# Performance work log

Hardware: AMD Instinct MI355X
Metric: run time of the kernel (lower is better)

## Reference

```python
import jax, jax.numpy as jnp
import numpy as np

EPS = 1e-5


def setup_inputs() -> dict:
    key = jax.random.key(0)
    k1, k2, k3 = jax.random.split(key, 3)
    B, D, T = 16, 256, 4096
    K = 2048
    x = jax.random.normal(k1, (B, D, T), dtype=jnp.float32)
    embedding_sum = jax.random.normal(k2, (K, D), dtype=jnp.float32)
    cluster_usage = jax.random.uniform(k3, (K,), dtype=jnp.float32)
    return {"x": x, "embedding_sum": embedding_sum, "cluster_usage": cluster_usage}


def reference(x, embedding_sum, cluster_usage):
    # embedding property: embedding_sum / clamp(cluster_usage, min=eps)
    emb = embedding_sum / jnp.clip(cluster_usage, EPS, None)[:, None]  # [K, D]
    B, D, T = x.shape
    x_flat = jnp.transpose(x, (0, 2, 1)).reshape(B * T, D)  # (b t) d
    # compute faithfully (clamped for numerical safety).
    x2 = jnp.sum(x_flat * x_flat, axis=-1, keepdims=True)      # [BT, 1]
    e2 = jnp.sum(emb * emb, axis=-1)                           # [K]
    d2 = x2 - 2.0 * (x_flat @ emb.T) + e2[None, :]             # [BT, K]
    distances = jnp.sqrt(jnp.clip(d2, 0.0, None))
    codes = jnp.argmin(distances, axis=-1).reshape(B, 1, T)    # int codes
    # decode: embedding gather, b t d -> b d t
    decoded = jnp.transpose(emb[codes[:, 0, :]], (0, 2, 1))    # [B, D, T]
    return codes, decoded
```

## Files before the change

kernel.cpp:

```cpp
#include <hip/hip_runtime.h>
#include <hip/hip_fp16.h>
#include <cmath>

#define EPS 1e-5f
#define TAU 0.15f
#define RP  8

#define Bn 16
#define Dn 256
#define Tn 4096
#define Kn 2048

typedef unsigned short ushort_t;
typedef __attribute__((ext_vector_type(8))) _Float16 f16x8;
typedef __attribute__((ext_vector_type(4))) float f32x4;

__device__ __forceinline__ unsigned short f2h(float v) {
    return __half_as_ushort(__float2half_rn(v));
}

#define GLOAD_LDS16(gp, lp) __builtin_amdgcn_global_load_lds( \
    (const __attribute__((address_space(1))) unsigned int*)(gp), \
    (__attribute__((address_space(3))) unsigned int*)(lp), 16, 0, 0)

__global__ __launch_bounds__(256) void prep_kernel(
    const float* __restrict__ es, const float* __restrict__ usage,
    float* __restrict__ emb, ushort_t* __restrict__ e16,
    float* __restrict__ bias, float4* __restrict__ embT4,
    int* __restrict__ counter)
{
    __shared__ float sh[256];
    __shared__ float wsum[4];
    const int k = blockIdx.x;
    const int d = threadIdx.x;
    const float inv = 1.0f / fmaxf(usage[k], EPS);
    const float v = es[(size_t)k * Dn + d] * inv;
    emb[(size_t)k * Dn + d] = v;
    e16[(size_t)k * Dn + d] = f2h(fminf(fmaxf(v, -65504.f), 65504.f));
    sh[d] = v;
    float sq = v * v;
    #pragma unroll
    for (int off = 32; off > 0; off >>= 1) sq += __shfl_down(sq, off, 64);
    const int lane = d & 63, wv = d >> 6;
    if (lane == 0) wsum[wv] = sq;
    __syncthreads();
    if (d < 64)
        embT4[(size_t)d * Kn + k] = make_float4(sh[4*d], sh[4*d+1], sh[4*d+2], sh[4*d+3]);
    if (d == 0) {
        bias[k] = 0.5f * (wsum[0] + wsum[1] + wsum[2] + wsum[3]);
        if (k == 0) *counter = 0;
    }
}

#define BARRIER_PIN()                                                         \
    __builtin_amdgcn_s_barrier();                                             \
    __builtin_amdgcn_sched_barrier(0)

#define STAGE_B(dst, kcc, hh)                                                 \
    {                                                                         \
        _Pragma("unroll")                                                     \
        for (int r = 0; r < 4; ++r) {                                         \
            const int c   = r * 512 + tid;                                    \
            const int row = c >> 4;                                           \
            const int col = (((c & 15) ^ (row & 15)) << 3);                   \
            GLOAD_LDS16(e16 + ((size_t)((kcc) * 128 + row)) * Dn + (hh) * 128 + col, \
                        (dst) + ((r * 512 + (wid << 6)) << 3));               \
        }                                                                     \
    }

#define COMPUTE_ACC(bbuf, afArr)                                              \
    {                                                                         \
        __builtin_amdgcn_s_setprio(1);                                        \
        _Pragma("unroll")                                                     \
        for (int ks = 0; ks < 4; ++ks)                                        \
            _Pragma("unroll")                                                 \
            for (int j = 0; j < 8; ++j) {                                     \
                const f16x8 bf = *(const f16x8*)(                             \
                    &(bbuf)[((j << 4) + l15) * 128 +                          \
                            ((((ks << 2) | quad) ^ l15) << 3)]);              \
                _Pragma("unroll")                                             \
                for (int i = 0; i < 2; ++i)                                   \
                    acc[i][j] = __builtin_amdgcn_mfma_f32_16x16x32_f16(       \
                        afArr[ks * 2 + i], bf, acc[i][j], 0, 0, 0);           \
            }                                                                 \
        __builtin_amdgcn_s_setprio(0);                                        \
    }

__global__ __launch_bounds__(512, 2) void gemm_argmax(
    const float* __restrict__ x, const ushort_t* __restrict__ e16,
    const float* __restrict__ bias_g, const float* __restrict__ emb,
    int* __restrict__ codes_i, float* __restrict__ codes_f,
    int* __restrict__ list, int* __restrict__ counter,
    float* __restrict__ decoded)
{
    __shared__ __align__(16) ushort_t BsS[2][128 * 128];
    __shared__ __align__(16) float    biasLds[2048];
    __shared__ int codeLds[256];

    const int bid = blockIdx.x;
    const int b   = bid >> 4;
    const int tt  = bid & 15;
    const int t0  = tt << 8;

    const int tid  = threadIdx.x;
    const int lane = tid & 63;
    const int wid  = tid >> 6;
    const int l15  = lane & 15;
    const int quad = lane >> 4;
    const int wm   = wid;

    const size_t bTt0 = (size_t)b * Tn + t0;

    GLOAD_LDS16(bias_g + (tid << 2), biasLds + (wid << 8));

    f16x8 af0[8], af1[8];
    {
        const float* xb = x + (size_t)b * Dn * Tn;
        #pragma unroll
        for (int ks = 0; ks < 4; ++ks)
            #pragma unroll
            for (int i = 0; i < 2; ++i) {
                const int t = t0 + (wm << 5) + (i << 4) + l15;
                const float* c0 = xb + ((size_t)(ks * 32 + quad * 8)) * Tn + t;
                const float* c1 = c0 + (size_t)128 * Tn;
                f16x8 v0, v1;
                #pragma unroll
                for (int e = 0; e < 8; ++e) {
                    v0[e] = (_Float16)c0[(size_t)e * Tn];
                    v1[e] = (_Float16)c1[(size_t)e * Tn];
                }
                af0[ks * 2 + i] = v0;
                af1[ks * 2 + i] = v1;
            }
    }

    f32x4 acc[2][8];
    float S1[2][4], S2[2][4];
    int   K1[2][4];
    #pragma unroll
    for (int i = 0; i < 2; ++i)
        #pragma unroll
        for (int r = 0; r < 4; ++r) { S1[i][r] = -INFINITY; S2[i][r] = -INFINITY; K1[i][r] = 0; }
    #pragma unroll
    for (int i = 0; i < 2; ++i)
        #pragma unroll
        for (int j = 0; j < 8; ++j)
            acc[i][j] = (f32x4){-INFINITY, -INFINITY, -INFINITY, -INFINITY};

    asm volatile("s_waitcnt vmcnt(0)" ::: "memory");
    BARRIER_PIN();
    STAGE_B(&BsS[0][0], 0, 0);
    STAGE_B(&BsS[1][0], 0, 1);

    #pragma unroll 1
    for (int kc = 0; kc < 16; ++kc) {
        asm volatile("s_waitcnt vmcnt(4)" ::: "memory");
        BARRIER_PIN();
        {
            float bj[8];
            #pragma unroll
            for (int j = 0; j < 8; ++j)
                bj[j] = biasLds[(kc << 7) + (j << 4) + l15];
            const int kdrb = ((kc - 1) << 7) + l15;
            __builtin_amdgcn_s_setprio(1);
            #pragma unroll
            for (int j = 0; j < 8; ++j) {
                const f16x8 bf0 = *(const f16x8*)(
                    &BsS[0][((j << 4) + l15) * 128 + ((quad ^ l15) << 3)]);
                const float nb = -bj[j];
                const f32x4 cin = {nb, nb, nb, nb};
                const int kdr = kdrb + (j << 4);
                #pragma unroll
                for (int i = 0; i < 2; ++i) {
                    #pragma unroll
                    for (int r = 0; r < 4; ++r) {
                        const float s = acc[i][j][r];
                        S2[i][r] = __builtin_amdgcn_fmed3f(s, S1[i][r], S2[i][r]);
                        const bool gt = s > S1[i][r];
                        K1[i][r] = gt ? kdr : K1[i][r];
                        S1[i][r] = fmaxf(S1[i][r], s);
                    }
                    acc[i][j] = __builtin_amdgcn_mfma_f32_16x16x32_f16(
                        af0[i], bf0, cin, 0, 0, 0);
                }
            }
            #pragma unroll
            for (int ks = 1; ks < 4; ++ks)
                #pragma unroll
                for (int j = 0; j < 8; ++j) {
                    const f16x8 bf = *(const f16x8*)(
                        &BsS[0][((j << 4) + l15) * 128 +
                                ((((ks << 2) | quad) ^ l15) << 3)]);
                    #pragma unroll
                    for (int i = 0; i < 2; ++i)
                        acc[i][j] = __builtin_amdgcn_mfma_f32_16x16x32_f16(
                            af0[ks * 2 + i], bf, acc[i][j], 0, 0, 0);
                }
            __builtin_amdgcn_s_setprio(0);
        }
        BARRIER_PIN();
        if (kc < 15) STAGE_B(&BsS[0][0], kc + 1, 0);

        if (kc < 15) { asm volatile("s_waitcnt vmcnt(4)" ::: "memory"); }
        else         { asm volatile("s_waitcnt vmcnt(0)" ::: "memory"); }
        BARRIER_PIN();
        COMPUTE_ACC((&BsS[1][0]), af1);
        BARRIER_PIN();
        if (kc < 15) STAGE_B(&BsS[1][0], kc + 1, 1);
    }

    __builtin_amdgcn_sched_barrier(0);

    {
        const int kfb = (15 << 7) + l15;
        #pragma unroll
        for (int j = 0; j < 8; ++j) {
            const int kf = kfb + (j << 4);
            #pragma unroll
            for (int i = 0; i < 2; ++i)
                #pragma unroll
                for (int r = 0; r < 4; ++r) {
                    const float s = acc[i][j][r];
                    S2[i][r] = __builtin_amdgcn_fmed3f(s, S1[i][r], S2[i][r]);
                    const bool gt = s > S1[i][r];
                    K1[i][r] = gt ? kf : K1[i][r];
                    S1[i][r] = fmaxf(S1[i][r], s);
                }
        }
    }

    #pragma unroll
    for (int m = 1; m <= 8; m <<= 1) {
        #pragma unroll
        for (int i = 0; i < 2; ++i)
            #pragma unroll
            for (int r = 0; r < 4; ++r) {
                const float os1 = __shfl_xor(S1[i][r], m);
                const float os2 = __shfl_xor(S2[i][r], m);
                const int   ok1 = __shfl_xor(K1[i][r], m);
                const bool take = (os1 > S1[i][r]) || (os1 == S1[i][r] && ok1 < K1[i][r]);
                const float ns2 = take ? fmaxf(S1[i][r], os2) : fmaxf(S2[i][r], os1);
                if (take) { S1[i][r] = os1; K1[i][r] = ok1; }
                S2[i][r] = ns2;
            }
    }

    if (l15 == 0) {
        #pragma unroll
        for (int i = 0; i < 2; ++i)
            #pragma unroll
            for (int r = 0; r < 4; ++r) {
                const int row = (wm << 5) + (i << 4) + (quad << 2) + r;
                const size_t p = bTt0 + row;
                const int wk = K1[i][r];
                codeLds[row] = wk;
                codes_i[p] = wk;
                codes_f[p] = (float)wk;
                if (S1[i][r] - S2[i][r] < TAU) {
                    const int idx = atomicAdd(counter, 1);
                    list[idx] = (int)p;
                }
            }
    }
    __syncthreads();

    {
        const int p2 = tid & 255;
        const int dh = tid >> 8;
        const int c  = codeLds[p2];
        const float4* e4 = (const float4*)(emb + (size_t)c * Dn) + dh * 32;
        float* ob = decoded + ((size_t)(b * Dn + dh * 128)) * Tn + t0 + p2;
        #pragma unroll 4
        for (int q = 0; q < 32; ++q) {
            const float4 v = e4[q];
            ob[(size_t)(q * 4 + 0) * Tn] = v.x;
            ob[(size_t)(q * 4 + 1) * Tn] = v.y;
            ob[(size_t)(q * 4 + 2) * Tn] = v.z;
            ob[(size_t)(q * 4 + 3) * Tn] = v.w;
        }
    }
}

__global__ __launch_bounds__(256) void rescue_kernel(
    const float* __restrict__ x, const float4* __restrict__ embT4,
    const float* __restrict__ bias, const float* __restrict__ emb,
    const int* __restrict__ list, const int* __restrict__ counter,
    int* __restrict__ codes_i, float* __restrict__ codes_f,
    float* __restrict__ decoded)
{
    __shared__ float xv[RP][256];
    __shared__ int plist[RP];
    __shared__ float rs[RP][4];
    __shared__ int   rk[RP][4];
    __shared__ int   fcode[RP];
    const int tid = threadIdx.x, lane = tid & 63, wid = tid >> 6;
    const int count = *counter;
    for (int base = blockIdx.x * RP; base < count; base += gridDim.x * RP) {
        const int npts = min(RP, count - base);
        __syncthreads();
        if (tid < npts) plist[tid] = list[base + tid];
        __syncthreads();
        for (int pi = 0; pi < npts; ++pi) {
            const int p = plist[pi];
            xv[pi][tid] = x[((size_t)((p >> 12) * Dn + tid)) * Tn + (p & 4095)];
        }
        for (int pi = npts; pi < RP; ++pi) xv[pi][tid] = 0.f;
        __syncthreads();

        float acc[8][RP];
        #pragma unroll
        for (int s = 0; s < 8; ++s)
            #pragma unroll
            for (int pi = 0; pi < RP; ++pi) acc[s][pi] = 0.f;

        for (int dc = 0; dc < 64; ++dc) {
            float4 ev[8];
            #pragma unroll
            for (int s = 0; s < 8; ++s)
                ev[s] = embT4[(size_t)dc * Kn + tid + (s << 8)];
            #pragma unroll
            for (int pi = 0; pi < RP; ++pi) {
                const float4 xw = *(const float4*)&xv[pi][dc << 2];
                #pragma unroll
                for (int s = 0; s < 8; ++s)
                    acc[s][pi] += ev[s].x * xw.x + ev[s].y * xw.y
                                + ev[s].z * xw.z + ev[s].w * xw.w;
            }
        }

        float bs[RP]; int bk[RP];
        #pragma unroll
        for (int pi = 0; pi < RP; ++pi) { bs[pi] = -INFINITY; bk[pi] = 0; }
        #pragma unroll
        for (int s = 0; s < 8; ++s) {
            const int kk = tid + (s << 8);
            const float bv = bias[kk];
            #pragma unroll
            for (int pi = 0; pi < RP; ++pi) {
                const float sc = acc[s][pi] - bv;
                if (sc > bs[pi]) { bs[pi] = sc; bk[pi] = kk; }
            }
        }
        #pragma unroll
        for (int off = 1; off < 64; off <<= 1) {
            #pragma unroll
            for (int pi = 0; pi < RP; ++pi) {
                const float os = __shfl_xor(bs[pi], off);
                const int   ok = __shfl_xor(bk[pi], off);
                if (os > bs[pi] || (os == bs[pi] && ok < bk[pi])) { bs[pi] = os; bk[pi] = ok; }
            }
        }
        if (lane == 0) {
            #pragma unroll
            for (int pi = 0; pi < RP; ++pi) { rs[pi][wid] = bs[pi]; rk[pi][wid] = bk[pi]; }
        }
        __syncthreads();
        if (tid < npts) {
            float fs = rs[tid][0]; int fk = rk[tid][0];
            #pragma unroll
            for (int w = 1; w < 4; ++w) {
                if (rs[tid][w] > fs || (rs[tid][w] == fs && rk[tid][w] < fk)) {
                    fs = rs[tid][w]; fk = rk[tid][w];
                }
            }
            const int p = plist[tid];
            codes_i[p] = fk;
            codes_f[p] = (float)fk;
            fcode[tid] = fk;
        }
        __syncthreads();
        for (int pi = 0; pi < npts; ++pi) {
            const int p = plist[pi];
            const int c = fcode[pi];
            decoded[((size_t)((p >> 12) * Dn + tid)) * Tn + (p & 4095)] =
                emb[(size_t)c * Dn + tid];
        }
    }
}

extern "C" void kernel_launch(void* const* d_in, const int* in_sizes, int n_in,
                              void* d_out, int out_size, void* d_ws, size_t ws_size,
                              hipStream_t stream) {
    const float* x     = (const float*)d_in[0];
    const float* es    = (const float*)d_in[1];
    const float* usage = (const float*)d_in[2];

    char* ws = (char*)d_ws;
    float*    emb     = (float*)(ws + 0);
    float*    bias    = (float*)(ws + 2097152);
    ushort_t* e16     = (ushort_t*)(ws + 2105344);
    float4*   embT4   = (float4*)(ws + 3153920);
    int*      codes_i = (int*)(ws + 5251072);
    int*      list    = (int*)(ws + 5513216);
    int*      counter = (int*)(ws + 5775360);

    float* codes_f = (float*)d_out;
    float* decoded = (float*)d_out + (size_t)Bn * Tn;

    prep_kernel<<<Kn, 256, 0, stream>>>(es, usage, emb, e16, bias, embT4, counter);

    gemm_argmax<<<256, 512, 0, stream>>>(x, e16, bias, emb, codes_i, codes_f,
                                         list, counter, decoded);

    rescue_kernel<<<1024, 256, 0, stream>>>(x, embT4, bias, emb, list, counter,
                                            codes_i, codes_f, decoded);
}
```

Measured before the change: 296.7 us.

## Rescue ambiguous points with fp16 MFMA candidate filter then exact fp32 rescoring

The rescue kernel used to compute full fp32 scores over all 2048 codes for each ambiguous point. It now runs an fp16 MFMA pass over 32 points per block to collect the codes whose approximate score comes within TAU of the main kernel's best score. Only those candidates are rescored in fp32, with a packed atomicMax that keeps ties resolved to the lowest index. If a point collects more than MAXC candidates it falls back to scanning every code. The transposed fp32 embedding copy in prep is dropped, removing its strided writes, at the cost of more shared-memory atomics and some reliance on fp16 error staying below TAU.

```diff
diff --git a/kernel.cpp b/kernel.cpp
--- a/kernel.cpp
+++ b/kernel.cpp
@@ -4,7 +4,8 @@
 
 #define EPS 1e-5f
 #define TAU 0.15f
-#define RP  8
+#define RQ  32
+#define MAXC 64
 
 #define Bn 16
 #define Dn 256
@@ -26,10 +27,8 @@
 __global__ __launch_bounds__(256) void prep_kernel(
     const float* __restrict__ es, const float* __restrict__ usage,
     float* __restrict__ emb, ushort_t* __restrict__ e16,
-    float* __restrict__ bias, float4* __restrict__ embT4,
-    int* __restrict__ counter)
+    float* __restrict__ bias, int* __restrict__ counter)
 {
-    __shared__ float sh[256];
     __shared__ float wsum[4];
     const int k = blockIdx.x;
     const int d = threadIdx.x;
@@ -37,15 +36,12 @@
     const float v = es[(size_t)k * Dn + d] * inv;
     emb[(size_t)k * Dn + d] = v;
     e16[(size_t)k * Dn + d] = f2h(fminf(fmaxf(v, -65504.f), 65504.f));
-    sh[d] = v;
     float sq = v * v;
     #pragma unroll
     for (int off = 32; off > 0; off >>= 1) sq += __shfl_down(sq, off, 64);
     const int lane = d & 63, wv = d >> 6;
     if (lane == 0) wsum[wv] = sq;
     __syncthreads();
-    if (d < 64)
-        embT4[(size_t)d * Kn + k] = make_float4(sh[4*d], sh[4*d+1], sh[4*d+2], sh[4*d+3]);
     if (d == 0) {
         bias[k] = 0.5f * (wsum[0] + wsum[1] + wsum[2] + wsum[3]);
         if (k == 0) *counter = 0;
@@ -90,8 +86,8 @@
     const float* __restrict__ x, const ushort_t* __restrict__ e16,
     const float* __restrict__ bias_g, const float* __restrict__ emb,
     int* __restrict__ codes_i, float* __restrict__ codes_f,
-    int* __restrict__ list, int* __restrict__ counter,
-    float* __restrict__ decoded)
+    int* __restrict__ list, float* __restrict__ slist,
+    int* __restrict__ counter, float* __restrict__ decoded)
 {
     __shared__ __align__(16) ushort_t BsS[2][128 * 128];
     __shared__ __align__(16) float    biasLds[2048];
@@ -258,7 +254,8 @@
                 codes_f[p] = (float)wk;
                 if (S1[i][r] - S2[i][r] < TAU) {
                     const int idx = atomicAdd(counter, 1);
-                    list[idx] = (int)p;
+                    list[idx]  = (int)p;
+                    slist[idx] = S1[i][r];
                 }
             }
     }
@@ -282,91 +279,120 @@
 }
 
 __global__ __launch_bounds__(256) void rescue_kernel(
-    const float* __restrict__ x, const float4* __restrict__ embT4,
+    const float* __restrict__ x, const ushort_t* __restrict__ e16,
     const float* __restrict__ bias, const float* __restrict__ emb,
-    const int* __restrict__ list, const int* __restrict__ counter,
-    int* __restrict__ codes_i, float* __restrict__ codes_f,
-    float* __restrict__ decoded)
+    const int* __restrict__ list, const float* __restrict__ slist,
+    const int* __restrict__ counter, int* __restrict__ codes_i,
+    float* __restrict__ codes_f, float* __restrict__ decoded)
 {
-    __shared__ float xv[RP][256];
-    __shared__ int plist[RP];
-    __shared__ float rs[RP][4];
-    __shared__ int   rk[RP][4];
-    __shared__ int   fcode[RP];
-    const int tid = threadIdx.x, lane = tid & 63, wid = tid >> 6;
+    __shared__ float    xv32[RQ][256];
+    __shared__ ushort_t xhs[RQ][256];
+    __shared__ int      cand[RQ][MAXC];
+    __shared__ int      ccnt[RQ];
+    __shared__ float    s1l[RQ];
+    __shared__ unsigned long long best[RQ];
+    __shared__ int      plist[RQ];
+    __shared__ int      fcode[RQ];
+
+    const int tid  = threadIdx.x;
+    const int lane = tid & 63;
+    const int wid  = tid >> 6;
+    const int l15  = lane & 15;
+    const int quad = lane >> 4;
     const int count = *counter;
-    for (int base = blockIdx.x * RP; base < count; base += gridDim.x * RP) {
-        const int npts = min(RP, count - base);
-        __syncthreads();
-        if (tid < npts) plist[tid] = list[base + tid];
+
+    for (int base = blockIdx.x * RQ; base < count; base += gridDim.x * RQ) {
+        const int npts = min(RQ, count - base);
+        __syncthreads();
+        if (tid < RQ) {
+            ccnt[tid] = 0;
+            best[tid] = 0ull;
+            if (tid < npts) { plist[tid] = list[base + tid]; s1l[tid] = slist[base + tid]; }
+            else            { plist[tid] = 0; s1l[tid] = INFINITY; }
+        }
         __syncthreads();
         for (int pi = 0; pi < npts; ++pi) {
             const int p = plist[pi];
-            xv[pi][tid] = x[((size_t)((p >> 12) * Dn + tid)) * Tn + (p & 4095)];
-        }
-        for (int pi = npts; pi < RP; ++pi) xv[pi][tid] = 0.f;
-        __syncthreads();
-
-        float acc[8][RP];
-        #pragma unroll
-        for (int s = 0; s < 8; ++s)
-            #pragma unroll
-            for (int pi = 0; pi < RP; ++pi) acc[s][pi] = 0.f;
-
-        for (int dc = 0; dc < 64; ++dc) {
-            float4 ev[8];
-            #pragma unroll
-            for (int s = 0; s < 8; ++s)
-                ev[s] = embT4[(size_t)dc * Kn + tid + (s << 8)];
-            #pragma unroll
-            for (int pi = 0; pi < RP; ++pi) {
-                const float4 xw = *(const float4*)&xv[pi][dc << 2];
-                #pragma unroll
-                for (int s = 0; s < 8; ++s)
-                    acc[s][pi] += ev[s].x * xw.x + ev[s].y * xw.y
-                                + ev[s].z * xw.z + ev[s].w * xw.w;
-            }
-        }
-
-        float bs[RP]; int bk[RP];
-        #pragma unroll
-        for (int pi = 0; pi < RP; ++pi) { bs[pi] = -INFINITY; bk[pi] = 0; }
-        #pragma unroll
-        for (int s = 0; s < 8; ++s) {
-            const int kk = tid + (s << 8);
-            const float bv = bias[kk];
-            #pragma unroll
-            for (int pi = 0; pi < RP; ++pi) {
-                const float sc = acc[s][pi] - bv;
-                if (sc > bs[pi]) { bs[pi] = sc; bk[pi] = kk; }
-            }
-        }
-        #pragma unroll
-        for (int off = 1; off < 64; off <<= 1) {
-            #pragma unroll
-            for (int pi = 0; pi < RP; ++pi) {
-                const float os = __shfl_xor(bs[pi], off);
-                const int   ok = __shfl_xor(bk[pi], off);
-                if (os > bs[pi] || (os == bs[pi] && ok < bk[pi])) { bs[pi] = os; bk[pi] = ok; }
-            }
-        }
-        if (lane == 0) {
-            #pragma unroll
-            for (int pi = 0; pi < RP; ++pi) { rs[pi][wid] = bs[pi]; rk[pi][wid] = bk[pi]; }
+            const float v = x[((size_t)((p >> 12) * Dn + tid)) * Tn + (p & 4095)];
+            xv32[pi][tid] = v;
+            xhs[pi][tid]  = __half_as_ushort(__float2half_rn(v));
+        }
+        for (int pi = npts; pi < RQ; ++pi) { xv32[pi][tid] = 0.f; xhs[pi][tid] = 0; }
+        __syncthreads();
+
+        f16x8 af[16];
+        #pragma unroll
+        for (int ds = 0; ds < 8; ++ds)
+            #pragma unroll
+            for (int i = 0; i < 2; ++i)
+                af[ds * 2 + i] = *(const f16x8*)(&xhs[i * 16 + l15][ds * 32 + quad * 8]);
+        float s1r[2][4];
+        #pragma unroll
+        for (int i = 0; i < 2; ++i)
+            #pragma unroll
+            for (int r = 0; r < 4; ++r)
+                s1r[i][r] = s1l[i * 16 + quad * 4 + r] - TAU;
+
+        const int kb = wid << 9;
+        for (int j = 0; j < 32; ++j) {
+            const int kj = kb + (j << 4);
+            const float nb = -bias[kj + l15];
+            f32x4 acc0 = {nb, nb, nb, nb};
+            f32x4 acc1 = {nb, nb, nb, nb};
+            #pragma unroll
+            for (int ds = 0; ds < 8; ++ds) {
+                const f16x8 bf = *(const f16x8*)(
+                    e16 + ((size_t)(kj + l15)) * Dn + ds * 32 + quad * 8);
+                acc0 = __builtin_amdgcn_mfma_f32_16x16x32_f16(af[ds * 2 + 0], bf, acc0, 0, 0, 0);
+                acc1 = __builtin_amdgcn_mfma_f32_16x16x32_f16(af[ds * 2 + 1], bf, acc1, 0, 0, 0);
+            }
+            const int kk = kj + l15;
+            #pragma unroll
+            for (int r = 0; r < 4; ++r) {
+                if (acc0[r] > s1r[0][r]) {
+                    const int pt = quad * 4 + r;
+                    const int ix = atomicAdd(&ccnt[pt], 1);
+                    if (ix < MAXC) cand[pt][ix] = kk;
+                }
+                if (acc1[r] > s1r[1][r]) {
+                    const int pt = 16 + quad * 4 + r;
+                    const int ix = atomicAdd(&ccnt[pt], 1);
+                    if (ix < MAXC) cand[pt][ix] = kk;
+                }
+            }
+        }
+        __syncthreads();
+
+        for (int pi = 0; pi < npts; ++pi) {
+            const int cc = ccnt[pi];
+            const int cn = (cc > MAXC) ? Kn : cc;
+            for (int c = wid; c < cn; c += 4) {
+                const int k = (cc > MAXC) ? c : cand[pi][c];
+                const float* er = emb + (size_t)k * Dn;
+                float s = 0.f;
+                #pragma unroll
+                for (int e = 0; e < 4; ++e)
+                    s += er[lane * 4 + e] * xv32[pi][lane * 4 + e];
+                #pragma unroll
+                for (int off = 32; off > 0; off >>= 1)
+                    s += __shfl_xor(s, off);
+                if (lane == 0) {
+                    s -= bias[k];
+                    unsigned sb = __float_as_uint(s);
+                    sb = (sb & 0x80000000u) ? ~sb : (sb | 0x80000000u);
+                    const unsigned long long pk =
+                        ((unsigned long long)sb << 32) | (unsigned)(2047 - k);
+                    atomicMax(&best[pi], pk);
+                }
+            }
         }
         __syncthreads();
         if (tid < npts) {
-            float fs = rs[tid][0]; int fk = rk[tid][0];
-            #pragma unroll
-            for (int w = 1; w < 4; ++w) {
-                if (rs[tid][w] > fs || (rs[tid][w] == fs && rk[tid][w] < fk)) {
-                    fs = rs[tid][w]; fk = rk[tid][w];
-                }
-            }
+            const int k = 2047 - (int)(best[tid] & 0xFFFFFFFFu);
+            fcode[tid] = k;
             const int p = plist[tid];
-            codes_i[p] = fk;
-            codes_f[p] = (float)fk;
-            fcode[tid] = fk;
+            codes_i[p] = k;
+            codes_f[p] = (float)k;
         }
         __syncthreads();
         for (int pi = 0; pi < npts; ++pi) {
@@ -389,19 +415,19 @@
     float*    emb     = (float*)(ws + 0);
     float*    bias    = (float*)(ws + 2097152);
     ushort_t* e16     = (ushort_t*)(ws + 2105344);
-    float4*   embT4   = (float4*)(ws + 3153920);
     int*      codes_i = (int*)(ws + 5251072);
     int*      list    = (int*)(ws + 5513216);
     int*      counter = (int*)(ws + 5775360);
+    float*    slist   = (float*)(ws + 5775376);
 
     float* codes_f = (float*)d_out;
     float* decoded = (float*)d_out + (size_t)Bn * Tn;
 
-    prep_kernel<<<Kn, 256, 0, stream>>>(es, usage, emb, e16, bias, embT4, counter);
+    prep_kernel<<<Kn, 256, 0, stream>>>(es, usage, emb, e16, bias, counter);
 
     gemm_argmax<<<256, 512, 0, stream>>>(x, e16, bias, emb, codes_i, codes_f,
-                                         list, counter, decoded);
-
-    rescue_kernel<<<1024, 256, 0, stream>>>(x, embT4, bias, emb, list, counter,
-                                            codes_i, codes_f, decoded);
+                                         list, slist, counter, decoded);
+
+    rescue_kernel<<<512, 256, 0, stream>>>(x, e16, bias, emb, list, slist,
+                                           counter, codes_i, codes_f, decoded);
 }
```

Measured after the change: 319.4 us. 1.08x slower.
